# Kernel tuning notes

Hardware: AMD Instinct MI355X
Metric: run time of the kernel (lower is better)

Reference implementation:

```python
import jax, jax.numpy as jnp
import numpy as np
from jax import lax

H = 145; W = 145; BANDS = 200; D_MODEL = 128; NUM_CLASSES = 17
# Mamba2 defaults: expand=2, headdim=64, d_state=128, d_conv=4, ngroups=1
D_INNER = 256; NHEADS = 4; HEADDIM = 64; D_STATE = 128; D_CONV = 4
D_IN_PROJ = 2 * D_INNER + 2 * D_STATE + NHEADS  # 772
CONV_DIM = D_INNER + 2 * D_STATE                # 512


def _gelu(x):
    return jax.nn.gelu(x, approximate=False)


def _ln(x, g, b, eps=1e-5):
    m = jnp.mean(x, -1, keepdims=True)
    v = jnp.mean((x - m) ** 2, -1, keepdims=True)
    return (x - m) * lax.rsqrt(v + eps) * g + b


def _adaptive_pool_last(x, out):
    # PyTorch AdaptiveAvgPool semantics along the last axis via integral image
    L = x.shape[-1]
    i = np.arange(out)
    starts = (i * L) // out
    ends = -((-(i + 1) * L) // out)  # ceil((i+1)*L/out)
    cs = jnp.concatenate([jnp.zeros(x.shape[:-1] + (1,), x.dtype), jnp.cumsum(x, -1)], -1)
    return (cs[..., ends] - cs[..., starts]) / jnp.asarray(ends - starts, x.dtype)


def _mamba2(u, in_w, conv_w, conv_b, dt_bias, A_log, D, norm_w, out_w):
    # u: (L, D_MODEL). Faithful Mamba2 reference path (batch=1 squeezed).
    L = u.shape[0]
    zxbcdt = u @ in_w                      # (L, 772)
    z = zxbcdt[:, :D_INNER]                # (L, 256)
    xBC = zxbcdt[:, D_INNER:2 * D_INNER + 2 * D_STATE]  # (L, 512)
    dt = jax.nn.softplus(zxbcdt[:, -NHEADS:] + dt_bias)  # (L, 4)
    # causal depthwise conv1d, kernel D_CONV, then SiLU
    xp = jnp.pad(xBC, ((D_CONV - 1, 0), (0, 0)))
    xBC = sum(xp[k:k + L] * conv_w[:, k] for k in range(D_CONV)) + conv_b
    xBC = jax.nn.silu(xBC)
    xh = xBC[:, :D_INNER].reshape(L, NHEADS, HEADDIM)     # (L, h, p)
    Bm = xBC[:, D_INNER:D_INNER + D_STATE]                # (L, n)
    Cm = xBC[:, D_INNER + D_STATE:]                       # (L, n)
    A = -jnp.exp(A_log)                                   # (h,)

    def step(state, inp):
        dt_t, x_t, B_t, C_t = inp          # (h,), (h,p), (n,), (n,)
        dA = jnp.exp(dt_t * A)             # (h,)
        state = state * dA[:, None, None] + (dt_t[:, None] * x_t)[:, :, None] * B_t[None, None, :]
        y_t = jnp.einsum('hpn,n->hp', state, C_t)
        return state, y_t

    s0 = jnp.zeros((NHEADS, HEADDIM, D_STATE), u.dtype)
    _, y = lax.scan(step, s0, (dt, xh, Bm, Cm))           # y: (L, h, p)
    y = y + D[None, :, None] * xh
    y = y.reshape(L, D_INNER) * jax.nn.silu(z)            # gated
    y = y * lax.rsqrt(jnp.mean(y * y, -1, keepdims=True) + 1e-5) * norm_w  # RMSNormGated
    return y @ out_w                                      # (L, D_MODEL)


def _forward(x, ln_pre_g, ln_pre_b, fe_w1, fe_b1, fe_w2, fe_b2,
             cv_w1, cv_b1, cv_w2, cv_b2, mp_w, mp_b, mp_ln_g, mp_ln_b,
             m_in_w, m_conv_w, m_conv_b, m_dt_bias, m_A_log, m_D, m_norm_w, m_out_w,
             cls_ln_g, cls_ln_b, cls_w1, cls_b1, cls_w2, cls_b2, cls_w3, cls_b3):
    h, w, _ = x.shape
    xn = _ln(x, ln_pre_g, ln_pre_b)
    # MLP feature branch
    f = _gelu(xn @ fe_w1 + fe_b1)
    f = _gelu(f @ fe_w2 + fe_b2)                          # (h, w, 128)
    # conv branch
    c = jnp.transpose(xn, (2, 0, 1))[None]                # (1, bands, h, w)
    dn = ('NCHW', 'OIHW', 'NCHW')
    c = lax.conv_general_dilated(c, cv_w1, (1, 1), [(2, 2), (2, 2)], dimension_numbers=dn)
    c = _gelu(c + cv_b1[None, :, None, None])             # (1, 32, 147, 147)
    c = lax.conv_general_dilated(c, cv_w2, (1, 1), [(1, 1), (1, 1)], dimension_numbers=dn)
    c = _gelu(c + cv_b2[None, :, None, None])             # (1, 64, 147, 147)
    c = _adaptive_pool_last(c, W)                         # pool width -> 145
    c = _adaptive_pool_last(c.swapaxes(-1, -2), H).swapaxes(-1, -2)  # pool height
    conv_feat = jnp.transpose(c[0], (1, 2, 0))            # (145, 145, 64)
    comb = jnp.concatenate([f, conv_feat], -1).reshape(h * w, 192)
    p = _gelu(_ln(comb @ mp_w + mp_b, mp_ln_g, mp_ln_b))  # (L, d_model)
    m = _mamba2(p, m_in_w, m_conv_w, m_conv_b, m_dt_bias, m_A_log, m_D, m_norm_w, m_out_w)
    r = m.reshape(h, w, D_MODEL)
    o = _ln(r, cls_ln_g, cls_ln_b)
    o = _gelu(o @ cls_w1 + cls_b1)
    o = _gelu(o @ cls_w2 + cls_b2)
    return o @ cls_w3 + cls_b3                            # (h, w, num_classes)


def setup_inputs() -> dict:
    key = jax.random.key(0)
    ks = jax.random.split(key, 16)
    def n(k, shape, s=0.02):
        return jax.random.normal(k, shape, jnp.float32) * s
    return dict(
        x=jax.random.normal(ks[0], (H, W, BANDS), jnp.float32),
        ln_pre_g=jnp.ones((BANDS,), jnp.float32), ln_pre_b=jnp.zeros((BANDS,), jnp.float32),
        fe_w1=n(ks[1], (BANDS, 256)), fe_b1=jnp.zeros((256,), jnp.float32),
        fe_w2=n(ks[2], (256, 128)), fe_b2=jnp.zeros((128,), jnp.float32),
        cv_w1=n(ks[3], (32, BANDS, 3, 3)), cv_b1=jnp.zeros((32,), jnp.float32),
        cv_w2=n(ks[4], (64, 32, 3, 3)), cv_b2=jnp.zeros((64,), jnp.float32),
        mp_w=n(ks[5], (192, D_MODEL)), mp_b=jnp.zeros((D_MODEL,), jnp.float32),
        mp_ln_g=jnp.ones((D_MODEL,), jnp.float32), mp_ln_b=jnp.zeros((D_MODEL,), jnp.float32),
        m_in_w=n(ks[6], (D_MODEL, D_IN_PROJ)),
        m_conv_w=n(ks[7], (CONV_DIM, D_CONV), 0.2), m_conv_b=jnp.zeros((CONV_DIM,), jnp.float32),
        m_dt_bias=jnp.full((NHEADS,), -4.0, jnp.float32),
        m_A_log=jnp.log(jnp.linspace(1.0, 16.0, NHEADS)).astype(jnp.float32),
        m_D=jnp.ones((NHEADS,), jnp.float32),
        m_norm_w=jnp.ones((D_INNER,), jnp.float32),
        m_out_w=n(ks[8], (D_INNER, D_MODEL)),
        cls_ln_g=jnp.ones((D_MODEL,), jnp.float32), cls_ln_b=jnp.zeros((D_MODEL,), jnp.float32),
        cls_w1=n(ks[9], (D_MODEL, 128)), cls_b1=jnp.zeros((128,), jnp.float32),
        cls_w2=n(ks[10], (128, 64)), cls_b2=jnp.zeros((64,), jnp.float32),
        cls_w3=n(ks[11], (64, NUM_CLASSES)), cls_b3=jnp.zeros((NUM_CLASSES,), jnp.float32),
    )


def reference(x, ln_pre_g, ln_pre_b, fe_w1, fe_b1, fe_w2, fe_b2,
              cv_w1, cv_b1, cv_w2, cv_b2, mp_w, mp_b, mp_ln_g, mp_ln_b,
              m_in_w, m_conv_w, m_conv_b, m_dt_bias, m_A_log, m_D, m_norm_w, m_out_w,
              cls_ln_g, cls_ln_b, cls_w1, cls_b1, cls_w2, cls_b2, cls_w3, cls_b3):
    return _forward(x, ln_pre_g, ln_pre_b, fe_w1, fe_b1, fe_w2, fe_b2,
                    cv_w1, cv_b1, cv_w2, cv_b2, mp_w, mp_b, mp_ln_g, mp_ln_b,
                    m_in_w, m_conv_w, m_conv_b, m_dt_bias, m_A_log, m_D, m_norm_w, m_out_w,
                    cls_ln_g, cls_ln_b, cls_w1, cls_b1, cls_w2, cls_b2, cls_w3, cls_b3)
```

## Files before the change

### kernel.cpp

```cpp
#include <hip/hip_runtime.h>
#include <math.h>

#define HW 21025
#define Hdim 145
#define Wdim 145
#define NBANDS 200
#define CONVH 147
#define CONVHW 21609
#define QC 64
#define NCH 329
#define DTP 21056
#define SP 72
#define SSD_GRID 1344

typedef __attribute__((ext_vector_type(4))) float fv4;
typedef __attribute__((ext_vector_type(8))) short short8;

#define OFF_XN   ((size_t)0)
#define OFF_F1   ((size_t)4205000)
#define OFF_COMB ((size_t)9587400)
#define OFF_P    ((size_t)13624200)
#define OFF_ZX   ((size_t)16315400)
#define OFF_XBC  ((size_t)32546700)
#define OFF_S    ((size_t)43311500)
#define OFF_DT   ((size_t)54092172)
#define OFF_CT   ((size_t)54176396)
#define OFF_W    ((size_t)54177712)

__device__ __forceinline__ float gelu_f(float x){
    return 0.5f * x * (1.0f + erff(x * 0.70710678118654752440f));
}
__device__ __forceinline__ float silu_f(float x){
    return x / (1.0f + expf(-x));
}

__device__ __forceinline__ void bf16_split(float x, unsigned short& hs, unsigned short& ls){
    unsigned u = __float_as_uint(x);
    hs = (unsigned short)(u >> 16);
    float hif = __uint_as_float(u & 0xFFFF0000u);
    float lof = x - hif;
    ls = (unsigned short)(__float_as_uint(lof) >> 16);
}
__device__ __forceinline__ unsigned pack2(unsigned short a, unsigned short b){
    return (unsigned)a | ((unsigned)b << 16);
}
__device__ __forceinline__ unsigned packsplit(float x){
    unsigned short hs, ls;
    bf16_split(x, hs, ls);
    return ((unsigned)hs << 16) | (unsigned)ls;
}
__device__ __forceinline__ float unpackf(unsigned u){
    return __uint_as_float(u & 0xFFFF0000u) + __uint_as_float(u << 16);
}
__device__ __forceinline__ void split8g(const float* p, short8& h8, short8& l8){
    fv4 v0 = *reinterpret_cast<const fv4*>(p);
    fv4 v1 = *reinterpret_cast<const fv4*>(p + 4);
    unsigned short hs, ls;
    #pragma unroll
    for (int j = 0; j < 4; j++){
        bf16_split(v0[j], hs, ls); h8[j] = (short)hs; l8[j] = (short)ls;
        bf16_split(v1[j], hs, ls); h8[4 + j] = (short)hs; l8[4 + j] = (short)ls;
    }
}
__device__ __forceinline__ void unpack8(const unsigned* p, short8& h8, short8& l8){
    uint4 a = *reinterpret_cast<const uint4*>(p);
    uint4 b = *reinterpret_cast<const uint4*>(p + 4);
    unsigned v0 = a.x, v1 = a.y, v2 = a.z, v3 = a.w;
    unsigned v4 = b.x, v5 = b.y, v6 = b.z, v7 = b.w;
    h8[0]=(short)(v0>>16); l8[0]=(short)(v0&0xFFFFu);
    h8[1]=(short)(v1>>16); l8[1]=(short)(v1&0xFFFFu);
    h8[2]=(short)(v2>>16); l8[2]=(short)(v2&0xFFFFu);
    h8[3]=(short)(v3>>16); l8[3]=(short)(v3&0xFFFFu);
    h8[4]=(short)(v4>>16); l8[4]=(short)(v4&0xFFFFu);
    h8[5]=(short)(v5>>16); l8[5]=(short)(v5&0xFFFFu);
    h8[6]=(short)(v6>>16); l8[6]=(short)(v6&0xFFFFu);
    h8[7]=(short)(v7>>16); l8[7]=(short)(v7&0xFFFFu);
}

template<int ACT>
__global__ void ln_kernel(const float* __restrict__ in, const float* __restrict__ g,
                          const float* __restrict__ b, float* __restrict__ out, int D){
    int row = blockIdx.x, tid = threadIdx.x;
    const float* r = in + (size_t)row * D;
    float s = 0.f, s2 = 0.f;
    for (int i = tid; i < D; i += 256){ float v = r[i]; s += v; s2 += v*v; }
    __shared__ float r1[4], r2[4];
    #pragma unroll
    for (int o = 32; o > 0; o >>= 1){ s += __shfl_down(s, o); s2 += __shfl_down(s2, o); }
    if ((tid & 63) == 0){ r1[tid >> 6] = s; r2[tid >> 6] = s2; }
    __syncthreads();
    float S = r1[0] + r1[1] + r1[2] + r1[3];
    float S2 = r2[0] + r2[1] + r2[2] + r2[3];
    float mean = S / (float)D;
    float var = S2 / (float)D - mean * mean;
    float rs = rsqrtf(fmaxf(var, 0.f) + 1e-5f);
    float* o_ = out + (size_t)row * D;
    for (int i = tid; i < D; i += 256){
        float v = (r[i] - mean) * rs * g[i] + b[i];
        if (ACT == 1) v = gelu_f(v);
        o_[i] = v;
    }
}

template<int ACT>
__global__ __launch_bounds__(256) void gemm_mfma(const float* __restrict__ A, int lda,
                                                 const float* __restrict__ B,
                                                 const float* __restrict__ bias,
                                                 float* __restrict__ C, int ldc,
                                                 int M, int N, int K){
    const int SA = 40;
    __shared__ __align__(16) unsigned short Ah[128 * SA], Al[128 * SA];
    __shared__ __align__(16) unsigned short Bh[64 * SA],  Bl[64 * SA];
    int tid = threadIdx.x;
    int lane = tid & 63, wid = tid >> 6;
    int wy = wid >> 1, wx = wid & 1;
    int bm = blockIdx.y * 128, bn = blockIdx.x * 64;
    int l15 = lane & 15, g = lane >> 4;

    fv4 acc[4][2];
    #pragma unroll
    for (int i = 0; i < 4; i++)
        #pragma unroll
        for (int j = 0; j < 2; j++) acc[i][j] = (fv4){0.f,0.f,0.f,0.f};

    int am = tid >> 1;
    int aq = (tid & 1) * 4;
    bool arow_ok = (bm + am) < M;
    int bn_t = tid & 63;
    int bk8 = (tid >> 6) * 8;
    bool bcol_ok = (bn + bn_t) < N;

    int nK = (K + 31) / 32;
    for (int ks = 0; ks < nK; ks++){
        int k0 = ks * 32;
        const float* Ap = A + (size_t)(bm + am) * lda + k0;
        #pragma unroll
        for (int f = 0; f < 4; f++){
            int kq = aq + f;
            fv4 v = (fv4){0.f,0.f,0.f,0.f};
            if (arow_ok && (k0 + kq * 4 + 4) <= K)
                v = *reinterpret_cast<const fv4*>(Ap + kq * 4);
            unsigned short hs[4], ls[4];
            #pragma unroll
            for (int j = 0; j < 4; j++) bf16_split(v[j], hs[j], ls[j]);
            unsigned off = am * SA + kq * 4;
            *reinterpret_cast<uint2*>(&Ah[off]) = make_uint2(pack2(hs[0],hs[1]), pack2(hs[2],hs[3]));
            *reinterpret_cast<uint2*>(&Al[off]) = make_uint2(pack2(ls[0],ls[1]), pack2(ls[2],ls[3]));
        }
        {
            unsigned short hs[8], ls[8];
            #pragma unroll
            for (int j = 0; j < 8; j++){
                int kk = k0 + bk8 + j;
                float v = (bcol_ok && kk < K) ? B[(size_t)kk * N + bn + bn_t] : 0.f;
                bf16_split(v, hs[j], ls[j]);
            }
            unsigned off = bn_t * SA + bk8;
            *reinterpret_cast<uint4*>(&Bh[off]) = make_uint4(pack2(hs[0],hs[1]), pack2(hs[2],hs[3]),
                                                             pack2(hs[4],hs[5]), pack2(hs[6],hs[7]));
            *reinterpret_cast<uint4*>(&Bl[off]) = make_uint4(pack2(ls[0],ls[1]), pack2(ls[2],ls[3]),
                                                             pack2(ls[4],ls[5]), pack2(ls[6],ls[7]));
        }
        __syncthreads();
        short8 afh[4], afl[4], bfh[2], bfl[2];
        #pragma unroll
        for (int mi = 0; mi < 4; mi++){
            unsigned off = (wy * 64 + mi * 16 + l15) * SA + g * 8;
            afh[mi] = *reinterpret_cast<const short8*>(&Ah[off]);
            afl[mi] = *reinterpret_cast<const short8*>(&Al[off]);
        }
        #pragma unroll
        for (int ni = 0; ni < 2; ni++){
            unsigned off = (wx * 32 + ni * 16 + l15) * SA + g * 8;
            bfh[ni] = *reinterpret_cast<const short8*>(&Bh[off]);
            bfl[ni] = *reinterpret_cast<const short8*>(&Bl[off]);
        }
        #pragma unroll
        for (int mi = 0; mi < 4; mi++)
            #pragma unroll
            for (int ni = 0; ni < 2; ni++){
                acc[mi][ni] = __builtin_amdgcn_mfma_f32_16x16x32_bf16(afh[mi], bfh[ni], acc[mi][ni], 0, 0, 0);
                acc[mi][ni] = __builtin_amdgcn_mfma_f32_16x16x32_bf16(afh[mi], bfl[ni], acc[mi][ni], 0, 0, 0);
                acc[mi][ni] = __builtin_amdgcn_mfma_f32_16x16x32_bf16(afl[mi], bfh[ni], acc[mi][ni], 0, 0, 0);
            }
        __syncthreads();
    }
    #pragma unroll
    for (int mi = 0; mi < 4; mi++){
        #pragma unroll
        for (int ni = 0; ni < 2; ni++){
            int cc = bn + wx * 32 + ni * 16 + l15;
            if (cc >= N) continue;
            float bv = bias ? bias[cc] : 0.f;
            #pragma unroll
            for (int j = 0; j < 4; j++){
                int rr = bm + wy * 64 + mi * 16 + g * 4 + j;
                if (rr >= M) continue;
                float v = acc[mi][ni][j] + bv;
                if (ACT == 1) v = gelu_f(v);
                C[(size_t)rr * ldc + cc] = v;
            }
        }
    }
}

template<int IC, int OC, int NCHUNK>
__global__ void prep_w(const float* __restrict__ w, unsigned short* __restrict__ Wh,
                       unsigned short* __restrict__ Wl){
    const int KP = NCHUNK * 288;
    int idx = blockIdx.x * 256 + threadIdx.x;
    if (idx >= OC * KP) return;
    int o = idx / KP, k = idx % KP;
    int ch = k / 288, rest = k % 288, t = rest / 32, c = rest & 31;
    int ci = ch * 32 + c;
    float v = (ci < IC) ? w[((size_t)o * IC + ci) * 9 + t] : 0.f;
    unsigned short hs, ls;
    bf16_split(v, hs, ls);
    Wh[idx] = hs; Wl[idx] = ls;
}

template<int IC, int OC, int PAD, int NCHUNK, int NFRAG>
__global__ __launch_bounds__(256) void conv_mfma(const float* __restrict__ in,
                                                 int inH, int inW,
                                                 const unsigned short* __restrict__ Wh,
                                                 const unsigned short* __restrict__ Wl,
                                                 const float* __restrict__ bias,
                                                 float* __restrict__ out){
    const int KP = NCHUNK * 288;
    const int CST = 40;
    __shared__ __align__(16) unsigned short Xh[3 * 68 * CST], Xl[3 * 68 * CST];
    int y = blockIdx.y;
    int x0 = blockIdx.x * 64;
    int tid = threadIdx.x;
    int lane = tid & 63, wid = tid >> 6;
    int wy = wid >> 1, wx = wid & 1;
    int l15 = lane & 15, g = lane >> 4;

    fv4 acc[2][NFRAG];
    #pragma unroll
    for (int mi = 0; mi < 2; mi++)
        #pragma unroll
        for (int ni = 0; ni < NFRAG; ni++) acc[mi][ni] = (fv4){0.f,0.f,0.f,0.f};

    for (int ch = 0; ch < NCHUNK; ch++){
        int ci0 = ch * 32;
        if (ch > 0) __syncthreads();
        for (int e = tid; e < 3 * 68 * 8; e += 256){
            int qd = e & 7;
            int c  = (e >> 3) % 68;
            int r  = e / 544;
            int iy = y - PAD + r, ix = x0 - PAD + c;
            fv4 v = (fv4){0.f,0.f,0.f,0.f};
            if ((unsigned)iy < (unsigned)inH && (unsigned)ix < (unsigned)inW &&
                (ci0 + qd * 4 + 4) <= IC)
                v = *reinterpret_cast<const fv4*>(in + ((size_t)iy * inW + ix) * IC + ci0 + qd * 4);
            unsigned short hs[4], ls[4];
            #pragma unroll
            for (int j = 0; j < 4; j++) bf16_split(v[j], hs[j], ls[j]);
            unsigned off = (r * 68 + c) * CST + qd * 4;
            *reinterpret_cast<uint2*>(&Xh[off]) = make_uint2(pack2(hs[0],hs[1]), pack2(hs[2],hs[3]));
            *reinterpret_cast<uint2*>(&Xl[off]) = make_uint2(pack2(ls[0],ls[1]), pack2(ls[2],ls[3]));
        }
        __syncthreads();
        #pragma unroll
        for (int t = 0; t < 9; t++){
            int ky = t / 3, kx = t % 3;
            short8 ah[2], al[2], bh[NFRAG], bl[NFRAG];
            #pragma unroll
            for (int mi = 0; mi < 2; mi++){
                unsigned off = (ky * 68 + wy * 32 + mi * 16 + l15 + kx) * CST + g * 8;
                ah[mi] = *reinterpret_cast<const short8*>(&Xh[off]);
                al[mi] = *reinterpret_cast<const short8*>(&Xl[off]);
            }
            #pragma unroll
            for (int ni = 0; ni < NFRAG; ni++){
                int oc = wx * (16 * NFRAG) + ni * 16 + l15;
                size_t woff = (size_t)oc * KP + ch * 288 + t * 32 + g * 8;
                bh[ni] = *reinterpret_cast<const short8*>(&Wh[woff]);
                bl[ni] = *reinterpret_cast<const short8*>(&Wl[woff]);
            }
            #pragma unroll
            for (int mi = 0; mi < 2; mi++)
                #pragma unroll
                for (int ni = 0; ni < NFRAG; ni++){
                    acc[mi][ni] = __builtin_amdgcn_mfma_f32_16x16x32_bf16(ah[mi], bh[ni], acc[mi][ni], 0, 0, 0);
                    acc[mi][ni] = __builtin_amdgcn_mfma_f32_16x16x32_bf16(ah[mi], bl[ni], acc[mi][ni], 0, 0, 0);
                    acc[mi][ni] = __builtin_amdgcn_mfma_f32_16x16x32_bf16(al[mi], bh[ni], acc[mi][ni], 0, 0, 0);
                }
        }
    }
    #pragma unroll
    for (int mi = 0; mi < 2; mi++)
        #pragma unroll
        for (int ni = 0; ni < NFRAG; ni++){
            int oc = wx * (16 * NFRAG) + ni * 16 + l15;
            float bv = bias[oc];
            #pragma unroll
            for (int j = 0; j < 4; j++){
                int x = x0 + wy * 32 + mi * 16 + g * 4 + j;
                if (x >= CONVH) continue;
                out[((size_t)y * CONVH + x) * OC + oc] = gelu_f(acc[mi][ni][j] + bv);
            }
        }
}

__global__ void pool_kernel(const float* __restrict__ c2, float* __restrict__ comb){
    int idx = blockIdx.x * 256 + threadIdx.x;
    if (idx >= HW * 64) return;
    int o = idx & 63;
    int pix = idx >> 6;
    int xo = pix % Wdim, yo = pix / Wdim;
    int ys = yo * CONVH / Hdim, ye = ((yo + 1) * CONVH + Hdim - 1) / Hdim;
    int xs = xo * CONVH / Wdim, xe = ((xo + 1) * CONVH + Wdim - 1) / Wdim;
    float s = 0.f;
    for (int yy = ys; yy < ye; yy++)
        for (int xx = xs; xx < xe; xx++)
            s += c2[((size_t)yy * CONVH + xx) * 64 + o];
    comb[(size_t)pix * 192 + 128 + o] = s / (float)((ye - ys) * (xe - xs));
}

__global__ void dt_kernel(const float* __restrict__ zx, const float* __restrict__ dt_bias,
                          float* __restrict__ dtbT){
    int t = blockIdx.x * 256 + threadIdx.x;
    int h = blockIdx.y;
    if (t >= HW) return;
    float v = zx[(size_t)t * 772 + 768 + h] + dt_bias[h];
    dtbT[h * DTP + t] = (v > 20.f) ? v : log1pf(expf(v));
}

__global__ __launch_bounds__(256) void conv1d_tiled(const float* __restrict__ zx,
                                                    const float* __restrict__ w,
                                                    const float* __restrict__ b,
                                                    float* __restrict__ xbc){
    __shared__ float xs[67 * 128];
    __shared__ float wc[4 * 128];
    __shared__ float bc[128];
    int t0 = blockIdx.y * 64;
    int c0 = blockIdx.x * 128;
    int tid = threadIdx.x;
    for (int e = tid; e < 67 * 128; e += 256){
        int rr = e >> 7, cc = e & 127;
        int t = t0 - 3 + rr;
        xs[e] = (t >= 0 && t < HW) ? zx[(size_t)t * 772 + 256 + c0 + cc] : 0.f;
    }
    if (tid < 128){
        bc[tid] = b[c0 + tid];
        #pragma unroll
        for (int k = 0; k < 4; k++) wc[k * 128 + tid] = w[(c0 + tid) * 4 + k];
    }
    __syncthreads();
    for (int e = tid; e < 64 * 128; e += 256){
        int tt = e >> 7, cc = e & 127;
        if (t0 + tt >= HW) continue;
        float acc = bc[cc];
        #pragma unroll
        for (int k = 0; k < 4; k++) acc += xs[(tt + k) * 128 + cc] * wc[k * 128 + cc];
        xbc[(size_t)(t0 + tt) * 512 + c0 + cc] = silu_f(acc);
    }
}

__device__ __forceinline__ void chunk_cumsum_t(const float* __restrict__ dtbT, int t0, int Q,
                                               int h, const float* __restrict__ A_log,
                                               float* cum, float* dth){
    int tid = threadIdx.x;
    if (tid < 64){
        float d = (tid < Q) ? dtbT[h * DTP + t0 + tid] : 0.f;
        dth[tid] = d;
        float A = -expf(A_log[h]);
        float a = d * A;
        #pragma unroll
        for (int off = 1; off < 64; off <<= 1){
            float u = __shfl_up(a, off);
            if (tid >= off) a += u;
        }
        cum[tid] = a;
    }
    __syncthreads();
}

__device__ __forceinline__ bool ssd_decode(int bid, int& c, int& h){
    int m = bid & 7, rest = bid >> 3;
    h = rest & 3;
    c = (rest >> 2) * 8 + m;
    return c < NCH;
}

__global__ __launch_bounds__(256) void ssd_phaseA(const float* __restrict__ xbc,
                                                  const float* __restrict__ dtbT,
                                                  const float* __restrict__ A_log,
                                                  unsigned* __restrict__ Sp,
                                                  float* __restrict__ chunkT){
    __shared__ __align__(16) unsigned short BTh[128 * SP], BTl[128 * SP];
    __shared__ __align__(16) unsigned short XTh[64 * SP],  XTl[64 * SP];
    __shared__ float cum[64], dth[64], wln[64];
    int c, h;
    if (!ssd_decode(blockIdx.x, c, h)) return;
    int t0 = c * QC, Q = min(QC, HW - t0);
    int tid = threadIdx.x;
    chunk_cumsum_t(dtbT, t0, Q, h, A_log, cum, dth);
    float T = cum[Q - 1];
    if (tid == 0) chunkT[c * 4 + h] = T;
    if (tid < 64) wln[tid] = (tid < Q) ? __expf(T - cum[tid]) * dth[tid] : 0.f;
    __syncthreads();
    for (int e2 = tid; e2 < 4096; e2 += 256){
        int nn = e2 & 127, sp = e2 >> 7;
        int s0 = 2 * sp;
        float v0 = (s0 < Q)     ? xbc[(size_t)(t0 + s0) * 512 + 256 + nn] : 0.f;
        float v1 = (s0 + 1 < Q) ? xbc[(size_t)(t0 + s0 + 1) * 512 + 256 + nn] : 0.f;
        unsigned short h0, l0, h1, l1;
        bf16_split(v0, h0, l0); bf16_split(v1, h1, l1);
        *reinterpret_cast<unsigned*>(&BTh[nn * SP + s0]) = pack2(h0, h1);
        *reinterpret_cast<unsigned*>(&BTl[nn * SP + s0]) = pack2(l0, l1);
    }
    for (int e2 = tid; e2 < 2048; e2 += 256){
        int pp = e2 & 63, sp = e2 >> 6;
        int s0 = 2 * sp;
        float v0 = (s0 < Q)     ? xbc[(size_t)(t0 + s0) * 512 + h * 64 + pp] * wln[s0] : 0.f;
        float v1 = (s0 + 1 < Q) ? xbc[(size_t)(t0 + s0 + 1) * 512 + h * 64 + pp] * wln[s0 + 1] : 0.f;
        unsigned short h0, l0, h1, l1;
        bf16_split(v0, h0, l0); bf16_split(v1, h1, l1);
        *reinterpret_cast<unsigned*>(&XTh[pp * SP + s0]) = pack2(h0, h1);
        *reinterpret_cast<unsigned*>(&XTl[pp * SP + s0]) = pack2(l0, l1);
    }
    __syncthreads();
    int lane = tid & 63, wid = tid >> 6;
    int wy = wid >> 1, wx = wid & 1;
    int l15 = lane & 15, g = lane >> 4;
    fv4 acc[2][4];
    #pragma unroll
    for (int mi = 0; mi < 2; mi++)
        #pragma unroll
        for (int ni = 0; ni < 4; ni++) acc[mi][ni] = (fv4){0.f,0.f,0.f,0.f};
    #pragma unroll
    for (int ks = 0; ks < 2; ks++){
        short8 ah[2], al[2], bh_[4], bl_[4];
        #pragma unroll
        for (int mi = 0; mi < 2; mi++){
            unsigned off = (wy * 32 + mi * 16 + l15) * SP + ks * 32 + g * 8;
            ah[mi] = *reinterpret_cast<const short8*>(&XTh[off]);
            al[mi] = *reinterpret_cast<const short8*>(&XTl[off]);
        }
        #pragma unroll
        for (int ni = 0; ni < 4; ni++){
            unsigned off = (wx * 64 + ni * 16 + l15) * SP + ks * 32 + g * 8;
            bh_[ni] = *reinterpret_cast<const short8*>(&BTh[off]);
            bl_[ni] = *reinterpret_cast<const short8*>(&BTl[off]);
        }
        #pragma unroll
        for (int mi = 0; mi < 2; mi++)
            #pragma unroll
            for (int ni = 0; ni < 4; ni++){
                acc[mi][ni] = __builtin_amdgcn_mfma_f32_16x16x32_bf16(ah[mi], bh_[ni], acc[mi][ni], 0, 0, 0);
                acc[mi][ni] = __builtin_amdgcn_mfma_f32_16x16x32_bf16(ah[mi], bl_[ni], acc[mi][ni], 0, 0, 0);
                acc[mi][ni] = __builtin_amdgcn_mfma_f32_16x16x32_bf16(al[mi], bh_[ni], acc[mi][ni], 0, 0, 0);
            }
    }
    size_t sb = (size_t)(c * 4 + h) * 8192;
    #pragma unroll
    for (int mi = 0; mi < 2; mi++)
        #pragma unroll
        for (int ni = 0; ni < 4; ni++)
            #pragma unroll
            for (int j = 0; j < 4; j++){
                int p = wy * 32 + mi * 16 + g * 4 + j;
                int n = wx * 64 + ni * 16 + l15;
                Sp[sb + p * 128 + n] = packsplit(acc[mi][ni][j]);
            }
}

__global__ __launch_bounds__(256) void ssd_phaseB(unsigned* __restrict__ Sp,
                                                  const float* __restrict__ chunkT){
    __shared__ float e[NCH];
    int tid = threadIdx.x;
    int idx = blockIdx.x * 256 + tid;
    int h = idx >> 13, pn = idx & 8191;
    for (int c = tid; c < NCH; c += 256) e[c] = __expf(chunkT[c * 4 + h]);
    __syncthreads();
    #define ADDR_(cc) Sp[((size_t)((cc) * 4 + h)) * 8192 + pn]
    unsigned r0 = ADDR_(0), r1 = ADDR_(1), r2 = ADDR_(2), r3 = ADDR_(3);
    float s = 0.f;
    int c = 0;
    for (; c + 8 <= NCH; c += 4){
        unsigned n0 = ADDR_(c + 4), n1 = ADDR_(c + 5), n2 = ADDR_(c + 6), n3 = ADDR_(c + 7);
        ADDR_(c) = packsplit(s);     s = fmaf(s, e[c],     unpackf(r0));
        ADDR_(c + 1) = packsplit(s); s = fmaf(s, e[c + 1], unpackf(r1));
        ADDR_(c + 2) = packsplit(s); s = fmaf(s, e[c + 2], unpackf(r2));
        ADDR_(c + 3) = packsplit(s); s = fmaf(s, e[c + 3], unpackf(r3));
        r0 = n0; r1 = n1; r2 = n2; r3 = n3;
    }
    for (; c < NCH; c++){
        unsigned nx = (c + 4 < NCH) ? ADDR_(c + 4) : 0u;
        float loc = unpackf(r0); r0 = r1; r1 = r2; r2 = r3; r3 = nx;
        ADDR_(c) = packsplit(s);
        s = fmaf(s, e[c], loc);
    }
    #undef ADDR_
}

__global__ __launch_bounds__(256) void ssd_phaseC(const float* __restrict__ xbc,
                                                  const float* __restrict__ dtbT,
                                                  const float* __restrict__ A_log,
                                                  const float* __restrict__ Dvec,
                                                  const unsigned* __restrict__ Sp,
                                                  float* __restrict__ y){
    __shared__ __align__(16) unsigned short U0h[64 * SP], U0l[64 * SP];
    __shared__ __align__(16) unsigned short U1h[64 * SP], U1l[64 * SP];
    __shared__ float cum[64], dth[64];
    int c, h;
    if (!ssd_decode(blockIdx.x, c, h)) return;
    int t0 = c * QC, Q = min(QC, HW - t0);
    int tid = threadIdx.x;
    chunk_cumsum_t(dtbT, t0, Q, h, A_log, cum, dth);
    int lane = tid & 63, wid = tid >> 6;
    int wy = wid >> 1, wx = wid & 1;
    int l15 = lane & 15, g = lane >> 4;

    int trow[2], srow[2], prow[2];
    #pragma unroll
    for (int i = 0; i < 2; i++){
        trow[i] = min(t0 + wy * 32 + i * 16 + l15, HW - 1);
        srow[i] = min(t0 + wx * 32 + i * 16 + l15, HW - 1);
        prow[i] = wx * 32 + i * 16 + l15;
    }

    fv4 accG[2][2], accA[2][2];
    #pragma unroll
    for (int mi = 0; mi < 2; mi++)
        #pragma unroll
        for (int ni = 0; ni < 2; ni++){ accG[mi][ni] = (fv4){0.f,0.f,0.f,0.f}; accA[mi][ni] = (fv4){0.f,0.f,0.f,0.f}; }

    const unsigned* Sbase = Sp + (size_t)(c * 4 + h) * 8192;
    #pragma unroll
    for (int k0 = 0; k0 < 128; k0 += 32){
        short8 ah[2], al[2], bh[2], bl[2], sh[2], sl[2];
        #pragma unroll
        for (int mi = 0; mi < 2; mi++)
            split8g(xbc + (size_t)trow[mi] * 512 + 384 + k0 + g * 8, ah[mi], al[mi]);
        #pragma unroll
        for (int ni = 0; ni < 2; ni++){
            split8g(xbc + (size_t)srow[ni] * 512 + 256 + k0 + g * 8, bh[ni], bl[ni]);
            unpack8(Sbase + prow[ni] * 128 + k0 + g * 8, sh[ni], sl[ni]);
        }
        #pragma unroll
        for (int mi = 0; mi < 2; mi++)
            #pragma unroll
            for (int ni = 0; ni < 2; ni++){
                accG[mi][ni] = __builtin_amdgcn_mfma_f32_16x16x32_bf16(ah[mi], bh[ni], accG[mi][ni], 0, 0, 0);
                accG[mi][ni] = __builtin_amdgcn_mfma_f32_16x16x32_bf16(ah[mi], bl[ni], accG[mi][ni], 0, 0, 0);
                accG[mi][ni] = __builtin_amdgcn_mfma_f32_16x16x32_bf16(al[mi], bh[ni], accG[mi][ni], 0, 0, 0);
                accA[mi][ni] = __builtin_amdgcn_mfma_f32_16x16x32_bf16(ah[mi], sh[ni], accA[mi][ni], 0, 0, 0);
                accA[mi][ni] = __builtin_amdgcn_mfma_f32_16x16x32_bf16(ah[mi], sl[ni], accA[mi][ni], 0, 0, 0);
                accA[mi][ni] = __builtin_amdgcn_mfma_f32_16x16x32_bf16(al[mi], sh[ni], accA[mi][ni], 0, 0, 0);
            }
    }
    #pragma unroll
    for (int mi = 0; mi < 2; mi++)
        #pragma unroll
        for (int ni = 0; ni < 2; ni++)
            #pragma unroll
            for (int j = 0; j < 4; j++){
                int t = wy * 32 + mi * 16 + g * 4 + j;
                int s = wx * 32 + ni * 16 + l15;
                float pv = 0.f;
                if (s <= t && s < Q)
                    pv = accG[mi][ni][j] * __expf(cum[t] - cum[s]) * dth[s];
                unsigned short hs, ls;
                bf16_split(pv, hs, ls);
                U0h[t * SP + s] = hs;
                U0l[t * SP + s] = ls;
            }
    for (int e2 = tid; e2 < 2048; e2 += 256){
        int pp = e2 & 63, sp = e2 >> 6;
        int s0 = 2 * sp;
        float v0 = (s0 < Q)     ? xbc[(size_t)(t0 + s0) * 512 + h * 64 + pp] : 0.f;
        float v1 = (s0 + 1 < Q) ? xbc[(size_t)(t0 + s0 + 1) * 512 + h * 64 + pp] : 0.f;
        unsigned short h0, l0, h1, l1;
        bf16_split(v0, h0, l0); bf16_split(v1, h1, l1);
        *reinterpret_cast<unsigned*>(&U1h[pp * SP + s0]) = pack2(h0, h1);
        *reinterpret_cast<unsigned*>(&U1l[pp * SP + s0]) = pack2(l0, l1);
    }
    __syncthreads();
    fv4 accY[2][2];
    #pragma unroll
    for (int mi = 0; mi < 2; mi++)
        #pragma unroll
        for (int ni = 0; ni < 2; ni++)
            #pragma unroll
            for (int j = 0; j < 4; j++){
                int t = wy * 32 + mi * 16 + g * 4 + j;
                accY[mi][ni][j] = __expf(cum[t]) * accA[mi][ni][j];
            }
    #pragma unroll
    for (int kk = 0; kk < 2; kk++){
        short8 ph[2], pl[2], xh[2], xl[2];
        #pragma unroll
        for (int mi = 0; mi < 2; mi++){
            unsigned off = (wy * 32 + mi * 16 + l15) * SP + kk * 32 + g * 8;
            ph[mi] = *reinterpret_cast<const short8*>(&U0h[off]);
            pl[mi] = *reinterpret_cast<const short8*>(&U0l[off]);
        }
        #pragma unroll
        for (int ni = 0; ni < 2; ni++){
            unsigned off = (wx * 32 + ni * 16 + l15) * SP + kk * 32 + g * 8;
            xh[ni] = *reinterpret_cast<const short8*>(&U1h[off]);
            xl[ni] = *reinterpret_cast<const short8*>(&U1l[off]);
        }
        #pragma unroll
        for (int mi = 0; mi < 2; mi++)
            #pragma unroll
            for (int ni = 0; ni < 2; ni++){
                accY[mi][ni] = __builtin_amdgcn_mfma_f32_16x16x32_bf16(ph[mi], xh[ni], accY[mi][ni], 0, 0, 0);
                accY[mi][ni] = __builtin_amdgcn_mfma_f32_16x16x32_bf16(ph[mi], xl[ni], accY[mi][ni], 0, 0, 0);
                accY[mi][ni] = __builtin_amdgcn_mfma_f32_16x16x32_bf16(pl[mi], xh[ni], accY[mi][ni], 0, 0, 0);
            }
    }
    float Dh = Dvec[h];
    #pragma unroll
    for (int mi = 0; mi < 2; mi++)
        #pragma unroll
        for (int ni = 0; ni < 2; ni++)
            #pragma unroll
            for (int j = 0; j < 4; j++){
                int t = wy * 32 + mi * 16 + g * 4 + j;
                if (t >= Q) continue;
                int p = wx * 32 + ni * 16 + l15;
                float xv = xbc[(size_t)(t0 + t) * 512 + h * 64 + p];
                y[(size_t)(t0 + t) * 256 + h * 64 + p] = accY[mi][ni][j] + Dh * xv;
            }
}

__global__ void gated_rms_kernel(float* __restrict__ y, const float* __restrict__ zx,
                                 const float* __restrict__ nw){
    int row = blockIdx.x, tid = threadIdx.x;
    float v = y[(size_t)row * 256 + tid];
    float z = zx[(size_t)row * 772 + tid];
    v *= silu_f(z);
    float s = v * v;
    __shared__ float r1[4];
    #pragma unroll
    for (int o = 32; o > 0; o >>= 1) s += __shfl_down(s, o);
    if ((tid & 63) == 0) r1[tid >> 6] = s;
    __syncthreads();
    float S = r1[0] + r1[1] + r1[2] + r1[3];
    float rs = rsqrtf(S / 256.f + 1e-5f);
    y[(size_t)row * 256 + tid] = v * rs * nw[tid];
}

extern "C" void kernel_launch(void* const* d_in, const int* in_sizes, int n_in,
                              void* d_out, int out_size, void* d_ws, size_t ws_size,
                              hipStream_t stream){
    (void)in_sizes; (void)n_in; (void)out_size; (void)ws_size;
    const float* x        = (const float*)d_in[0];
    const float* ln_pre_g = (const float*)d_in[1];
    const float* ln_pre_b = (const float*)d_in[2];
    const float* fe_w1    = (const float*)d_in[3];
    const float* fe_b1    = (const float*)d_in[4];
    const float* fe_w2    = (const float*)d_in[5];
    const float* fe_b2    = (const float*)d_in[6];
    const float* cv_w1    = (const float*)d_in[7];
    const float* cv_b1    = (const float*)d_in[8];
    const float* cv_w2    = (const float*)d_in[9];
    const float* cv_b2    = (const float*)d_in[10];
    const float* mp_w     = (const float*)d_in[11];
    const float* mp_b     = (const float*)d_in[12];
    const float* mp_ln_g  = (const float*)d_in[13];
    const float* mp_ln_b  = (const float*)d_in[14];
    const float* m_in_w   = (const float*)d_in[15];
    const float* m_conv_w = (const float*)d_in[16];
    const float* m_conv_b = (const float*)d_in[17];
    const float* m_dtb    = (const float*)d_in[18];
    const float* m_A_log  = (const float*)d_in[19];
    const float* m_D      = (const float*)d_in[20];
    const float* m_norm_w = (const float*)d_in[21];
    const float* m_out_w  = (const float*)d_in[22];
    const float* cls_ln_g = (const float*)d_in[23];
    const float* cls_ln_b = (const float*)d_in[24];
    const float* cls_w1   = (const float*)d_in[25];
    const float* cls_b1   = (const float*)d_in[26];
    const float* cls_w2   = (const float*)d_in[27];
    const float* cls_b2   = (const float*)d_in[28];
    const float* cls_w3   = (const float*)d_in[29];
    const float* cls_b3   = (const float*)d_in[30];

    float* ws   = (float*)d_ws;
    float* xn   = ws + OFF_XN;
    float* f1   = ws + OFF_F1;
    float* comb = ws + OFF_COMB;
    float* p    = ws + OFF_P;
    float* zx   = ws + OFF_ZX;
    float* xbc  = ws + OFF_XBC;
    unsigned* Sp = (unsigned*)(ws + OFF_S);
    float* dtbT = ws + OFF_DT;
    float* chkT = ws + OFF_CT;
    float* c1h  = ws + OFF_XBC;
    float* c2h  = ws + OFF_XBC + 691488;
    float* pr   = ws + OFF_XN;
    float* ybuf = ws + OFF_F1;
    float* mo   = ws + OFF_COMB;
    float* cls0 = ws + OFF_XN;
    float* cls1 = ws + OFF_P;
    float* cls2 = ws + OFF_COMB + 2691200;
    unsigned short* W1h = (unsigned short*)(ws + OFF_W);
    unsigned short* W1l = (unsigned short*)(ws + OFF_W + 32256);
    unsigned short* W2h = (unsigned short*)(ws + OFF_W + 64512);
    unsigned short* W2l = (unsigned short*)(ws + OFF_W + 73728);

    prep_w<200, 32, 7><<<(32 * 2016 + 255) / 256, 256, 0, stream>>>(cv_w1, W1h, W1l);
    prep_w<32, 64, 1><<<(64 * 288 + 255) / 256, 256, 0, stream>>>(cv_w2, W2h, W2l);
    ln_kernel<0><<<HW, 256, 0, stream>>>(x, ln_pre_g, ln_pre_b, xn, NBANDS);
    gemm_mfma<1><<<dim3(4, 165), 256, 0, stream>>>(xn, 200, fe_w1, fe_b1, f1, 256, HW, 256, 200);
    gemm_mfma<1><<<dim3(2, 165), 256, 0, stream>>>(f1, 256, fe_w2, fe_b2, comb, 192, HW, 128, 256);
    conv_mfma<200, 32, 2, 7, 1><<<dim3(3, CONVH), 256, 0, stream>>>(xn, Hdim, Wdim, W1h, W1l, cv_b1, c1h);
    conv_mfma<32, 64, 1, 1, 2><<<dim3(3, CONVH), 256, 0, stream>>>(c1h, CONVH, CONVH, W2h, W2l, cv_b2, c2h);
    pool_kernel<<<(HW * 64 + 255) / 256, 256, 0, stream>>>(c2h, comb);
    gemm_mfma<0><<<dim3(2, 165), 256, 0, stream>>>(comb, 192, mp_w, mp_b, pr, 128, HW, 128, 192);
    ln_kernel<1><<<HW, 256, 0, stream>>>(pr, mp_ln_g, mp_ln_b, p, 128);
    gemm_mfma<0><<<dim3(13, 165), 256, 0, stream>>>(p, 128, m_in_w, (const float*)nullptr, zx, 772, HW, 772, 128);
    dt_kernel<<<dim3((HW + 255) / 256, 4), 256, 0, stream>>>(zx, m_dtb, dtbT);
    conv1d_tiled<<<dim3(4, NCH), 256, 0, stream>>>(zx, m_conv_w, m_conv_b, xbc);
    ssd_phaseA<<<SSD_GRID, 256, 0, stream>>>(xbc, dtbT, m_A_log, Sp, chkT);
    ssd_phaseB<<<128, 256, 0, stream>>>(Sp, chkT);
    ssd_phaseC<<<SSD_GRID, 256, 0, stream>>>(xbc, dtbT, m_A_log, m_D, Sp, ybuf);
    gated_rms_kernel<<<HW, 256, 0, stream>>>(ybuf, zx, m_norm_w);
    gemm_mfma<0><<<dim3(2, 165), 256, 0, stream>>>(ybuf, 256, m_out_w, (const float*)nullptr, mo, 128, HW, 128, 256);
    ln_kernel<0><<<HW, 256, 0, stream>>>(mo, cls_ln_g, cls_ln_b, cls0, 128);
    gemm_mfma<1><<<dim3(2, 165), 256, 0, stream>>>(cls0, 128, cls_w1, cls_b1, cls1, 128, HW, 128, 128);
    gemm_mfma<1><<<dim3(1, 165), 256, 0, stream>>>(cls1, 128, cls_w2, cls_b2, cls2, 64, HW, 64, 128);
    gemm_mfma<0><<<dim3(1, 165), 256, 0, stream>>>(cls2, 64, cls_w3, cls_b3, (float*)d_out, 17, HW, 17, 64);
}
```

Measured before the change: 518.5 us.

## Store conv1d output pre-split as bf16 hi/lo and swizzle GEMM block order

The conv1d kernel now writes its SiLU output already split into packed bf16 high/low halves. The SSD phase A and C kernels therefore load these words directly instead of re-splitting fp32 values on every read, and unpack to float where a real value is needed. Separately, every GEMM launch uses a 1D grid with an XCD-style decode that groups 8 consecutive row-blocks together, aiming at better L2 locality across chiplets. The packed path depends on packsplit and unpackf being defined and on unpacking being accurate enough where plain floats are needed.

```diff
diff --git a/kernel.cpp b/kernel.cpp
--- a/kernel.cpp
+++ b/kernel.cpp
@@ -12,6 +12,7 @@
 #define DTP 21056
 #define SP 72
 #define SSD_GRID 1344
+#define NYB165 165
 
 typedef __attribute__((ext_vector_type(4))) float fv4;
 typedef __attribute__((ext_vector_type(8))) short short8;
@@ -77,6 +78,15 @@
     h8[7]=(short)(v7>>16); l8[7]=(short)(v7&0xFFFFu);
 }
 
+__device__ __forceinline__ bool gemm_decode(int bid, int NXB, int NYB, int& bx, int& by){
+    int m = bid & 7;
+    int r = bid >> 3;
+    bx = r % NXB;
+    by = (r / NXB) * 8 + m;
+    return by < NYB;
+}
+__host__ __forceinline__ int gemm_grid(int NXB, int NYB){ return 8 * ((NYB + 7) / 8) * NXB; }
+
 template<int ACT>
 __global__ void ln_kernel(const float* __restrict__ in, const float* __restrict__ g,
                           const float* __restrict__ b, float* __restrict__ out, int D){
@@ -107,14 +117,16 @@
                                                  const float* __restrict__ B,
                                                  const float* __restrict__ bias,
                                                  float* __restrict__ C, int ldc,
-                                                 int M, int N, int K){
+                                                 int M, int N, int K, int NXB, int NYB){
     const int SA = 40;
     __shared__ __align__(16) unsigned short Ah[128 * SA], Al[128 * SA];
     __shared__ __align__(16) unsigned short Bh[64 * SA],  Bl[64 * SA];
+    int bx, by;
+    if (!gemm_decode(blockIdx.x, NXB, NYB, bx, by)) return;
     int tid = threadIdx.x;
     int lane = tid & 63, wid = tid >> 6;
     int wy = wid >> 1, wx = wid & 1;
-    int bm = blockIdx.y * 128, bn = blockIdx.x * 64;
+    int bm = by * 128, bn = bx * 64;
     int l15 = lane & 15, g = lane >> 4;
 
     fv4 acc[4][2];
@@ -331,7 +343,7 @@
 __global__ __launch_bounds__(256) void conv1d_tiled(const float* __restrict__ zx,
                                                     const float* __restrict__ w,
                                                     const float* __restrict__ b,
-                                                    float* __restrict__ xbc){
+                                                    unsigned* __restrict__ xbcp){
     __shared__ float xs[67 * 128];
     __shared__ float wc[4 * 128];
     __shared__ float bc[128];
@@ -355,7 +367,7 @@
         float acc = bc[cc];
         #pragma unroll
         for (int k = 0; k < 4; k++) acc += xs[(tt + k) * 128 + cc] * wc[k * 128 + cc];
-        xbc[(size_t)(t0 + tt) * 512 + c0 + cc] = silu_f(acc);
+        xbcp[(size_t)(t0 + tt) * 512 + c0 + cc] = packsplit(silu_f(acc));
     }
 }
 
@@ -385,7 +397,7 @@
     return c < NCH;
 }
 
-__global__ __launch_bounds__(256) void ssd_phaseA(const float* __restrict__ xbc,
+__global__ __launch_bounds__(256) void ssd_phaseA(const unsigned* __restrict__ xbcp,
                                                   const float* __restrict__ dtbT,
                                                   const float* __restrict__ A_log,
                                                   unsigned* __restrict__ Sp,
@@ -405,18 +417,16 @@
     for (int e2 = tid; e2 < 4096; e2 += 256){
         int nn = e2 & 127, sp = e2 >> 7;
         int s0 = 2 * sp;
-        float v0 = (s0 < Q)     ? xbc[(size_t)(t0 + s0) * 512 + 256 + nn] : 0.f;
-        float v1 = (s0 + 1 < Q) ? xbc[(size_t)(t0 + s0 + 1) * 512 + 256 + nn] : 0.f;
-        unsigned short h0, l0, h1, l1;
-        bf16_split(v0, h0, l0); bf16_split(v1, h1, l1);
-        *reinterpret_cast<unsigned*>(&BTh[nn * SP + s0]) = pack2(h0, h1);
-        *reinterpret_cast<unsigned*>(&BTl[nn * SP + s0]) = pack2(l0, l1);
+        unsigned v0 = (s0 < Q)     ? xbcp[(size_t)(t0 + s0) * 512 + 256 + nn] : 0u;
+        unsigned v1 = (s0 + 1 < Q) ? xbcp[(size_t)(t0 + s0 + 1) * 512 + 256 + nn] : 0u;
+        *reinterpret_cast<unsigned*>(&BTh[nn * SP + s0]) = pack2((unsigned short)(v0 >> 16), (unsigned short)(v1 >> 16));
+        *reinterpret_cast<unsigned*>(&BTl[nn * SP + s0]) = pack2((unsigned short)(v0 & 0xFFFFu), (unsigned short)(v1 & 0xFFFFu));
     }
     for (int e2 = tid; e2 < 2048; e2 += 256){
         int pp = e2 & 63, sp = e2 >> 6;
         int s0 = 2 * sp;
-        float v0 = (s0 < Q)     ? xbc[(size_t)(t0 + s0) * 512 + h * 64 + pp] * wln[s0] : 0.f;
-        float v1 = (s0 + 1 < Q) ? xbc[(size_t)(t0 + s0 + 1) * 512 + h * 64 + pp] * wln[s0 + 1] : 0.f;
+        float v0 = (s0 < Q)     ? unpackf(xbcp[(size_t)(t0 + s0) * 512 + h * 64 + pp]) * wln[s0] : 0.f;
+        float v1 = (s0 + 1 < Q) ? unpackf(xbcp[(size_t)(t0 + s0 + 1) * 512 + h * 64 + pp]) * wln[s0 + 1] : 0.f;
         unsigned short h0, l0, h1, l1;
         bf16_split(v0, h0, l0); bf16_split(v1, h1, l1);
         *reinterpret_cast<unsigned*>(&XTh[pp * SP + s0]) = pack2(h0, h1);
@@ -497,7 +507,7 @@
     #undef ADDR_
 }
 
-__global__ __launch_bounds__(256) void ssd_phaseC(const float* __restrict__ xbc,
+__global__ __launch_bounds__(256) void ssd_phaseC(const unsigned* __restrict__ xbcp,
                                                   const float* __restrict__ dtbT,
                                                   const float* __restrict__ A_log,
                                                   const float* __restrict__ Dvec,
@@ -535,10 +545,10 @@
         short8 ah[2], al[2], bh[2], bl[2], sh[2], sl[2];
         #pragma unroll
         for (int mi = 0; mi < 2; mi++)
-            split8g(xbc + (size_t)trow[mi] * 512 + 384 + k0 + g * 8, ah[mi], al[mi]);
+            unpack8(xbcp + (size_t)trow[mi] * 512 + 384 + k0 + g * 8, ah[mi], al[mi]);
         #pragma unroll
         for (int ni = 0; ni < 2; ni++){
-            split8g(xbc + (size_t)srow[ni] * 512 + 256 + k0 + g * 8, bh[ni], bl[ni]);
+            unpack8(xbcp + (size_t)srow[ni] * 512 + 256 + k0 + g * 8, bh[ni], bl[ni]);
             unpack8(Sbase + prow[ni] * 128 + k0 + g * 8, sh[ni], sl[ni]);
         }
         #pragma unroll
@@ -572,12 +582,10 @@
     for (int e2 = tid; e2 < 2048; e2 += 256){
         int pp = e2 & 63, sp = e2 >> 6;
         int s0 = 2 * sp;
-        float v0 = (s0 < Q)     ? xbc[(size_t)(t0 + s0) * 512 + h * 64 + pp] : 0.f;
-        float v1 = (s0 + 1 < Q) ? xbc[(size_t)(t0 + s0 + 1) * 512 + h * 64 + pp] : 0.f;
-        unsigned short h0, l0, h1, l1;
-        bf16_split(v0, h0, l0); bf16_split(v1, h1, l1);
-        *reinterpret_cast<unsigned*>(&U1h[pp * SP + s0]) = pack2(h0, h1);
-        *reinterpret_cast<unsigned*>(&U1l[pp * SP + s0]) = pack2(l0, l1);
+        unsigned v0 = (s0 < Q)     ? xbcp[(size_t)(t0 + s0) * 512 + h * 64 + pp] : 0u;
+        unsigned v1 = (s0 + 1 < Q) ? xbcp[(size_t)(t0 + s0 + 1) * 512 + h * 64 + pp] : 0u;
+        *reinterpret_cast<unsigned*>(&U1h[pp * SP + s0]) = pack2((unsigned short)(v0 >> 16), (unsigned short)(v1 >> 16));
+        *reinterpret_cast<unsigned*>(&U1l[pp * SP + s0]) = pack2((unsigned short)(v0 & 0xFFFFu), (unsigned short)(v1 & 0xFFFFu));
     }
     __syncthreads();
     fv4 accY[2][2];
@@ -624,7 +632,7 @@
                 int t = wy * 32 + mi * 16 + g * 4 + j;
                 if (t >= Q) continue;
                 int p = wx * 32 + ni * 16 + l15;
-                float xv = xbc[(size_t)(t0 + t) * 512 + h * 64 + p];
+                float xv = unpackf(xbcp[(size_t)(t0 + t) * 512 + h * 64 + p]);
                 y[(size_t)(t0 + t) * 256 + h * 64 + p] = accY[mi][ni][j] + Dh * xv;
             }
 }
@@ -688,7 +696,7 @@
     float* comb = ws + OFF_COMB;
     float* p    = ws + OFF_P;
     float* zx   = ws + OFF_ZX;
-    float* xbc  = ws + OFF_XBC;
+    unsigned* xbcp = (unsigned*)(ws + OFF_XBC);
     unsigned* Sp = (unsigned*)(ws + OFF_S);
     float* dtbT = ws + OFF_DT;
     float* chkT = ws + OFF_CT;
@@ -708,23 +716,23 @@
     prep_w<200, 32, 7><<<(32 * 2016 + 255) / 256, 256, 0, stream>>>(cv_w1, W1h, W1l);
     prep_w<32, 64, 1><<<(64 * 288 + 255) / 256, 256, 0, stream>>>(cv_w2, W2h, W2l);
     ln_kernel<0><<<HW, 256, 0, stream>>>(x, ln_pre_g, ln_pre_b, xn, NBANDS);
-    gemm_mfma<1><<<dim3(4, 165), 256, 0, stream>>>(xn, 200, fe_w1, fe_b1, f1, 256, HW, 256, 200);
-    gemm_mfma<1><<<dim3(2, 165), 256, 0, stream>>>(f1, 256, fe_w2, fe_b2, comb, 192, HW, 128, 256);
+    gemm_mfma<1><<<gemm_grid(4, NYB165), 256, 0, stream>>>(xn, 200, fe_w1, fe_b1, f1, 256, HW, 256, 200, 4, NYB165);
+    gemm_mfma<1><<<gemm_grid(2, NYB165), 256, 0, stream>>>(f1, 256, fe_w2, fe_b2, comb, 192, HW, 128, 256, 2, NYB165);
     conv_mfma<200, 32, 2, 7, 1><<<dim3(3, CONVH), 256, 0, stream>>>(xn, Hdim, Wdim, W1h, W1l, cv_b1, c1h);
     conv_mfma<32, 64, 1, 1, 2><<<dim3(3, CONVH), 256, 0, stream>>>(c1h, CONVH, CONVH, W2h, W2l, cv_b2, c2h);
     pool_kernel<<<(HW * 64 + 255) / 256, 256, 0, stream>>>(c2h, comb);
-    gemm_mfma<0><<<dim3(2, 165), 256, 0, stream>>>(comb, 192, mp_w, mp_b, pr, 128, HW, 128, 192);
+    gemm_mfma<0><<<gemm_grid(2, NYB165), 256, 0, stream>>>(comb, 192, mp_w, mp_b, pr, 128, HW, 128, 192, 2, NYB165);
     ln_kernel<1><<<HW, 256, 0, stream>>>(pr, mp_ln_g, mp_ln_b, p, 128);
-    gemm_mfma<0><<<dim3(13, 165), 256, 0, stream>>>(p, 128, m_in_w, (const float*)nullptr, zx, 772, HW, 772, 128);
+    gemm_mfma<0><<<gemm_grid(13, NYB165), 256, 0, stream>>>(p, 128, m_in_w, (const float*)nullptr, zx, 772, HW, 772, 128, 13, NYB165);
     dt_kernel<<<dim3((HW + 255) / 256, 4), 256, 0, stream>>>(zx, m_dtb, dtbT);
-    conv1d_tiled<<<dim3(4, NCH), 256, 0, stream>>>(zx, m_conv_w, m_conv_b, xbc);
-    ssd_phaseA<<<SSD_GRID, 256, 0, stream>>>(xbc, dtbT, m_A_log, Sp, chkT);
+    conv1d_tiled<<<dim3(4, NCH), 256, 0, stream>>>(zx, m_conv_w, m_conv_b, xbcp);
+    ssd_phaseA<<<SSD_GRID, 256, 0, stream>>>(xbcp, dtbT, m_A_log, Sp, chkT);
     ssd_phaseB<<<128, 256, 0, stream>>>(Sp, chkT);
-    ssd_phaseC<<<SSD_GRID, 256, 0, stream>>>(xbc, dtbT, m_A_log, m_D, Sp, ybuf);
+    ssd_phaseC<<<SSD_GRID, 256, 0, stream>>>(xbcp, dtbT, m_A_log, m_D, Sp, ybuf);
     gated_rms_kernel<<<HW, 256, 0, stream>>>(ybuf, zx, m_norm_w);
-    gemm_mfma<0><<<dim3(2, 165), 256, 0, stream>>>(ybuf, 256, m_out_w, (const float*)nullptr, mo, 128, HW, 128, 256);
+    gemm_mfma<0><<<gemm_grid(2, NYB165), 256, 0, stream>>>(ybuf, 256, m_out_w, (const float*)nullptr, mo, 128, HW, 128, 256, 2, NYB165);
     ln_kernel<0><<<HW, 256, 0, stream>>>(mo, cls_ln_g, cls_ln_b, cls0, 128);
-    gemm_mfma<1><<<dim3(2, 165), 256, 0, stream>>>(cls0, 128, cls_w1, cls_b1, cls1, 128, HW, 128, 128);
-    gemm_mfma<1><<<dim3(1, 165), 256, 0, stream>>>(cls1, 128, cls_w2, cls_b2, cls2, 64, HW, 64, 128);
-    gemm_mfma<0><<<dim3(1, 165), 256, 0, stream>>>(cls2, 64, cls_w3, cls_b3, (float*)d_out, 17, HW, 17, 64);
-}
+    gemm_mfma<1><<<gemm_grid(2, NYB165), 256, 0, stream>>>(cls0, 128, cls_w1, cls_b1, cls1, 128, HW, 128, 128, 2, NYB165);
+    gemm_mfma<1><<<gemm_grid(1, NYB165), 256, 0, stream>>>(cls1, 128, cls_w2, cls_b2, cls2, 64, HW, 64, 128, 1, NYB165);
+    gemm_mfma<0><<<gemm_grid(1, NYB165), 256, 0, stream>>>(cls2, 64, cls_w3, cls_b3, (float*)d_out, 17, HW, 17, 64, 1, NYB165);
+}
```

Result: faster. 504.1 us (-2.8%).
